# Optimization experiments

Measured on AMD Instinct MI355X. Metric: run time of the kernel, lower is better.

## Reference

```python
import jax, jax.numpy as jnp
import numpy as np

EPS = 1e-8
CUTOFF = 7.0
B, A, EPG = 128, 100, 2048
N, E = B * A, B * EPG
LAT, HID, FCH, NRBF, NTYPES, NT = 256, 128, 512, 16, 100, 50


def _lattice(lengths, angles):
    # pymatgen-style lattice_params_to_matrix; angles in degrees. -> [B,3,3] rows are a,b,c vectors
    a, b, c = lengths[:, 0], lengths[:, 1], lengths[:, 2]
    al, be, ga = (jnp.radians(angles[:, k]) for k in range(3))
    val = (jnp.cos(al) * jnp.cos(be) - jnp.cos(ga)) / (jnp.sin(al) * jnp.sin(be))
    gs = jnp.arccos(jnp.clip(val, -1.0, 1.0))
    z = jnp.zeros_like(a)
    va = jnp.stack([a * jnp.sin(be), z, a * jnp.cos(be)], -1)
    vb = jnp.stack([-b * jnp.sin(al) * jnp.cos(gs), b * jnp.sin(al) * jnp.sin(gs), b * jnp.cos(al)], -1)
    vc = jnp.stack([z, z, c], -1)
    return jnp.stack([va, vb, vc], 1)


def setup_inputs() -> dict:
    rng = np.random.default_rng(0)
    # sorted-per-graph edge list with i != j (so no_iden_mask is all-true)
    i = rng.integers(0, A, (B, EPG))
    j = (i + rng.integers(1, A, (B, EPG))) % A
    order = np.argsort(i * A + j, axis=1, kind='stable')
    i = np.take_along_axis(i, order, 1)
    j = np.take_along_axis(j, order, 1)
    goff = (np.arange(B) * A)[:, None]
    edge_index = np.stack([(j + goff).reshape(-1), (i + goff).reshape(-1)]).astype(np.int32)  # [2,E], row0=j(src), row1=i(dst)
    to_jimages = rng.integers(-1, 2, (E, 3)).astype(np.int32)
    batch = np.repeat(np.arange(B), A).astype(np.int32)
    num_atoms = np.full((B,), A, np.int32)
    atom_types = rng.integers(0, NTYPES, (N,)).astype(np.int32)
    time_steps = rng.integers(0, NT, (B,)).astype(np.int32)

    ks = jax.random.split(jax.random.key(0), 12)
    f32 = jnp.float32
    inp = dict(
        latents=jax.random.normal(ks[0], (B, LAT), f32),
        gt_frac_coords=jax.random.uniform(ks[1], (N, 3), f32),
        lengths=8.0 + 4.0 * jax.random.uniform(ks[2], (B, 3), f32),
        angles=90.0 + 8.0 * (jax.random.uniform(ks[3], (B, 3), f32) - 0.5),
        coord_noise=jax.random.normal(ks[4], (N, 3), f32),
        sigmas=jnp.exp(jnp.linspace(np.log(0.01), np.log(10.0), NT)).astype(f32),
        atom_emb=jax.random.normal(ks[5], (NTYPES, HID), f32),
        rbf_W=0.05 * jax.random.normal(ks[6], (NRBF, HID), f32),
        rbf_b=jnp.zeros((HID,), f32),
        bb_W=0.1 * jax.random.normal(ks[7], (HID, HID), f32),
        bb_b=jnp.zeros((HID,), f32),
        sc_W0=0.05 * jax.random.normal(ks[8], (LAT + HID, FCH), f32),
        sc_b0=jnp.zeros((FCH,), f32),
        sc_W1=0.05 * jax.random.normal(ks[9], (FCH, FCH), f32),
        sc_b1=jnp.zeros((FCH,), f32),
        sc_W2=0.05 * jax.random.normal(ks[10], (FCH, 1), f32),
        sc_b2=jnp.zeros((1,), f32),
        num_atoms=jnp.asarray(num_atoms),
        atom_types=jnp.asarray(atom_types),
        batch=jnp.asarray(batch),
        edge_index=jnp.asarray(edge_index),
        to_jimages=jnp.asarray(to_jimages),
        time_steps=jnp.asarray(time_steps),
    )
    return inp


def reference(latents, gt_frac_coords, lengths, angles, coord_noise, sigmas,
              atom_emb, rbf_W, rbf_b, bb_W, bb_b,
              sc_W0, sc_b0, sc_W1, sc_b1, sc_W2, sc_b2,
              num_atoms, atom_types, batch, edge_index, to_jimages, time_steps):
    seg_sum = jax.ops.segment_sum
    L = _lattice(lengths, angles)            # [B,3,3]
    Linv = jnp.linalg.inv(L)
    Ln, Lni = L[batch], Linv[batch]          # per-node lattice [N,3,3]
    cart_gt = jnp.einsum('ni,nij->nj', gt_frac_coords, Ln)
    sig_node = sigmas[time_steps][batch][:, None]              # [N,1]
    pert = cart_gt + sig_node * coord_noise
    # correct_cart_coords: wrap back into unit cell
    frac_p = jnp.einsum('ni,nij->nj', pert, Lni) % 1.0
    pert = jnp.einsum('ni,nij->nj', frac_p, Ln)
    jn, iN = edge_index[0], edge_index[1]
    offs = jnp.einsum('ei,eij->ej', to_jimages.astype(pert.dtype), L[batch[jn]])
    dvec = pert[iN] - pert[jn] - offs                           # [E,3]
    dist = jnp.linalg.norm(dvec, axis=-1)
    # backbone: atom-type embeddings + Gaussian RBF edge MLP -> [E,HID]
    mus = jnp.linspace(0.0, CUTOFF, rbf_W.shape[0]).astype(pert.dtype)
    rbf = jnp.exp(-10.0 * (dist[:, None] - mus) ** 2)
    h = atom_emb[atom_types]
    ef = jax.nn.silu((h[jn] + h[iN] + rbf @ rbf_W + rbf_b) @ bb_W + bb_b)
    # latents repeat_interleave(num_multi_edge_per_graph) == gather by edge's graph id
    ef = jnp.concatenate([ef, latents[batch[jn]]], axis=1)      # [E, HID+LAT]
    hh = jax.nn.relu(ef @ sc_W0 + sc_b0)
    hh = jax.nn.relu(hh @ sc_W1 + sc_b1)
    scores = hh @ sc_W2 + sc_b2                                 # [E,1]
    # align_gt_cart_coords: minimum-image gt coords relative to perturbed coords
    frac_gt = jnp.einsum('ni,nij->nj', cart_gt, Lni)
    fd = frac_gt - frac_p
    fd = fd - jnp.round(fd)
    aligned = pert + jnp.einsum('ni,nij->nj', fd, Ln)
    gt_dvec = aligned[iN] - aligned[jn] - offs
    gt_d = jnp.linalg.norm(gt_dvec, axis=-1, keepdims=True)
    pd = dist[:, None]
    gt_scores = gt_d - pd
    # per_node loss: group multi-edges by contiguous (i,j) runs
    start = jnp.concatenate([jnp.ones((1,), bool), (iN[1:] != iN[:-1]) | (jn[1:] != jn[:-1])])
    seg = jnp.cumsum(start.astype(jnp.int32)) - 1               # [E], < E segments
    cnt = seg_sum(jnp.ones((E,), pert.dtype), seg, num_segments=E)
    c = jnp.maximum(cnt, 1.0)
    sv = scores * dvec / (pd + EPS)
    gv = gt_scores * dvec / (pd + EPS)
    sE = seg_sum(sv, seg, num_segments=E) / c[:, None]
    gE = seg_sum(gv, seg, num_segments=E) / c[:, None]
    recv = jnp.round(seg_sum(iN.astype(pert.dtype), seg, num_segments=E) / c).astype(jnp.int32)
    sN = seg_sum(sE, recv, num_segments=N)                      # scores_per_node_pos [N,3]
    gN = seg_sum(gE, recv, num_segments=N)
    sq = (sN - gN / sig_node) ** 2
    na = num_atoms.astype(pert.dtype)[:, None]
    score_loss = (seg_sum(sq, batch, num_segments=B) / na).mean()
    # pbc symmetry regularizer
    preds = pert + sN / sig_node
    center = seg_sum(preds, batch, num_segments=B) / na
    dc = preds - center[batch]
    pbs = (jnp.abs(dc[:, 0].max() + dc[:, 0].min())
           + jnp.abs(dc[:, 1].max() + dc[:, 1].min())
           + jnp.abs(dc[:, 2].max() + dc[:, 2].min()))
    return (score_loss, pbs)
```

## Files before the change

kernel.cpp:

```cpp
#include <hip/hip_runtime.h>
#include <hip/hip_bf16.h>

namespace {
constexpr int Bb = 128, Nn = 12800, Ee = 262144;
constexpr int LAT = 256, HID = 128, FCH = 512, NRBF = 16;
constexpr int TE = 64;
constexpr int TSTRIDE = 1040;

constexpr int WS_L      = 0;
constexpr int WS_LI     = 1152;
constexpr int WS_SIG    = 2304;
constexpr int WS_RBFW2  = 2432;
constexpr int WS_CVEC   = 4480;
constexpr int WS_HB     = 4608;
constexpr int WS_LATP   = 17408;
constexpr int WS_PERT   = 82944;
constexpr int WS_ALIGN  = 121344;
constexpr int WS_SN     = 159744;
constexpr int WS_GN     = 198144;
constexpr int WS_PREDS  = 236544;
constexpr int WS_BSUM   = 274944;
constexpr int WS_CENTER = 275328;
constexpr int WS_MINMAX = 275712;
constexpr int WS_W0T_F  = 276000;
constexpr int WS_W1T_F  = 308768;
}

typedef short bf16x8 __attribute__((ext_vector_type(8)));
typedef float f32x4 __attribute__((ext_vector_type(4)));

static __device__ __forceinline__ unsigned short f2bf(float f) {
  unsigned int u = __float_as_uint(f);
  unsigned int r = (u + 0x7fffu + ((u >> 16) & 1u)) >> 16;
  return (unsigned short)r;
}
static __device__ __forceinline__ unsigned int pk2bf(float a, float b) {
  unsigned int r;
  asm("v_cvt_pk_bf16_f32 %0, %1, %2" : "=v"(r) : "v"(a), "v"(b));
  return r;
}
static __device__ __forceinline__ float fastrcp(float x) {
  return __builtin_amdgcn_rcpf(x);
}

static __device__ __forceinline__ void atomicMaxFloat(float* addr, float val) {
  int* ai = reinterpret_cast<int*>(addr);
  int old = *ai;
  while (__int_as_float(old) < val) {
    int assumed = old;
    old = atomicCAS(ai, assumed, __float_as_int(val));
    if (old == assumed) break;
  }
}
static __device__ __forceinline__ void atomicMinFloat(float* addr, float val) {
  int* ai = reinterpret_cast<int*>(addr);
  int old = *ai;
  while (__int_as_float(old) > val) {
    int assumed = old;
    old = atomicCAS(ai, assumed, __float_as_int(val));
    if (old == assumed) break;
  }
}

__global__ __launch_bounds__(256) void k_pre(
    const float* lengths, const float* angles, const float* sigmas, const int* tsteps,
    const float* aemb, const float* bbW, const float* rbfW, const float* rbfb,
    const float* bbb, const float* latents, const float* scW0, const float* scb0,
    const float* scW1, unsigned short* w0t, unsigned short* w1t, float* ws) {
  const int blk = blockIdx.x, t = threadIdx.x;
  if (blk < 304) {
    int gid = blk * 256 + t;
    if (gid < 2 * Nn * 3) ws[WS_SN + gid] = 0.f;
    else if (gid < 2 * Nn * 3 + 2 * Bb * 3) ws[WS_BSUM + (gid - 2 * Nn * 3)] = 0.f;
    else if (gid < 2 * Nn * 3 + 2 * Bb * 3 + 3) ws[WS_MINMAX + (gid - 2 * Nn * 3 - 2 * Bb * 3)] = -3.0e38f;
    else if (gid < 2 * Nn * 3 + 2 * Bb * 3 + 6) ws[WS_MINMAX + (gid - 2 * Nn * 3 - 2 * Bb * 3)] = 3.0e38f;
  } else if (blk == 304) {
    int b = t;
    if (b >= Bb) return;
    float a = lengths[b * 3 + 0], bl = lengths[b * 3 + 1], c = lengths[b * 3 + 2];
    const float d2r = 0.017453292519943295f;
    float al = angles[b * 3 + 0] * d2r, be = angles[b * 3 + 1] * d2r, ga = angles[b * 3 + 2] * d2r;
    float ca = cosf(al), cb = cosf(be), cg = cosf(ga), sa = sinf(al), sb = sinf(be);
    float val = (ca * cb - cg) / (sa * sb);
    val = fminf(1.f, fmaxf(-1.f, val));
    float gs = acosf(val);
    float L[3][3];
    L[0][0] = a * sb;              L[0][1] = 0.f;                L[0][2] = a * cb;
    L[1][0] = -bl * sa * cosf(gs); L[1][1] = bl * sa * sinf(gs); L[1][2] = bl * ca;
    L[2][0] = 0.f;                 L[2][1] = 0.f;                L[2][2] = c;
    float det = L[0][0] * (L[1][1] * L[2][2] - L[1][2] * L[2][1])
              - L[0][1] * (L[1][0] * L[2][2] - L[1][2] * L[2][0])
              + L[0][2] * (L[1][0] * L[2][1] - L[1][1] * L[2][0]);
    float id = 1.f / det;
    float inv[3][3];
    inv[0][0] =  (L[1][1]*L[2][2] - L[1][2]*L[2][1]) * id;
    inv[0][1] = -(L[0][1]*L[2][2] - L[0][2]*L[2][1]) * id;
    inv[0][2] =  (L[0][1]*L[1][2] - L[0][2]*L[1][1]) * id;
    inv[1][0] = -(L[1][0]*L[2][2] - L[1][2]*L[2][0]) * id;
    inv[1][1] =  (L[0][0]*L[2][2] - L[0][2]*L[2][0]) * id;
    inv[1][2] = -(L[0][0]*L[1][2] - L[0][2]*L[1][0]) * id;
    inv[2][0] =  (L[1][0]*L[2][1] - L[1][1]*L[2][0]) * id;
    inv[2][1] = -(L[0][0]*L[2][1] - L[0][1]*L[2][0]) * id;
    inv[2][2] =  (L[0][0]*L[1][1] - L[0][1]*L[1][0]) * id;
    for (int i = 0; i < 3; ++i)
      for (int j = 0; j < 3; ++j) {
        ws[WS_L + b * 9 + i * 3 + j] = L[i][j];
        ws[WS_LI + b * 9 + i * 3 + j] = inv[i][j];
      }
    ws[WS_SIG + b] = sigmas[tsteps[b]];
  } else if (blk < 405) {
    int tile = blk - 305;
    if (t < HID) {
      float acc = 0.f;
      for (int k = 0; k < HID; ++k) acc += aemb[tile * HID + k] * bbW[k * HID + t];
      ws[WS_HB + tile * HID + t] = acc;
    }
  } else if (blk == 405) {
    if (t < HID) {
      float accs[NRBF];
#pragma unroll
      for (int k = 0; k < NRBF; ++k) accs[k] = 0.f;
      float accb = 0.f;
      for (int m = 0; m < HID; ++m) {
        float w = bbW[m * HID + t];
#pragma unroll
        for (int k = 0; k < NRBF; ++k) accs[k] += rbfW[k * HID + m] * w;
        accb += rbfb[m] * w;
      }
#pragma unroll
      for (int k = 0; k < NRBF; ++k) ws[WS_RBFW2 + k * HID + t] = accs[k];
      ws[WS_CVEC + t] = accb + bbb[t];
    }
  } else if (blk < 534) {
    int b = blk - 406;
    __shared__ float lat[LAT];
    lat[t] = latents[b * LAT + t];
    __syncthreads();
    int c0 = 2 * t;
    float a0 = 0.f, a1 = 0.f;
    for (int m = 0; m < LAT; ++m) {
      float2 w = *reinterpret_cast<const float2*>(scW0 + (HID + m) * FCH + c0);
      float lm = lat[m];
      a0 += lm * w.x;
      a1 += lm * w.y;
    }
    ws[WS_LATP + b * FCH + c0] = a0 + scb0[c0];
    ws[WS_LATP + b * FCH + c0 + 1] = a1 + scb0[c0 + 1];
  } else if (blk < 790) {
    int tid = (blk - 534) * 256 + t;
    int col = tid & 511, k = tid >> 9;
    int id = (((col >> 4) * 4 + (k >> 5)) * 64 + ((k & 31) >> 3) * 16 + (col & 15)) * 8 + (k & 7);
    w0t[id] = f2bf(scW0[tid]);
  } else {
    int tid = (blk - 790) * 256 + t;
    int col = tid & 511, k = tid >> 9;
    int id = (((col >> 4) * 16 + (k >> 5)) * 64 + ((k & 31) >> 3) * 16 + (col & 15)) * 8 + (k & 7);
    w1t[id] = f2bf(scW1[tid]);
  }
}

__global__ void k_node(const float* frac, const float* noise, const int* batch, float* ws) {
  int n = blockIdx.x * blockDim.x + threadIdx.x;
  if (n >= Nn) return;
  int b = batch[n];
  float L[9], Li[9];
#pragma unroll
  for (int i = 0; i < 9; ++i) { L[i] = ws[WS_L + b * 9 + i]; Li[i] = ws[WS_LI + b * 9 + i]; }
  float f0 = frac[n * 3], f1 = frac[n * 3 + 1], f2 = frac[n * 3 + 2];
  float cg[3], p0[3], fp[3], pe[3], fg[3], fd[3];
#pragma unroll
  for (int j = 0; j < 3; ++j) cg[j] = f0 * L[j] + f1 * L[3 + j] + f2 * L[6 + j];
  float sig = ws[WS_SIG + b];
#pragma unroll
  for (int j = 0; j < 3; ++j) p0[j] = cg[j] + sig * noise[n * 3 + j];
#pragma unroll
  for (int j = 0; j < 3; ++j) {
    float v = p0[0] * Li[j] + p0[1] * Li[3 + j] + p0[2] * Li[6 + j];
    fp[j] = v - floorf(v);
  }
#pragma unroll
  for (int j = 0; j < 3; ++j) pe[j] = fp[0] * L[j] + fp[1] * L[3 + j] + fp[2] * L[6 + j];
#pragma unroll
  for (int j = 0; j < 3; ++j) fg[j] = cg[0] * Li[j] + cg[1] * Li[3 + j] + cg[2] * Li[6 + j];
#pragma unroll
  for (int j = 0; j < 3; ++j) { float d = fg[j] - fp[j]; fd[j] = d - rintf(d); }
#pragma unroll
  for (int j = 0; j < 3; ++j) {
    ws[WS_PERT + n * 3 + j] = pe[j];
    ws[WS_ALIGN + n * 3 + j] = pe[j] + fd[0] * L[j] + fd[1] * L[3 + j] + fd[2] * L[6 + j];
  }
}

__global__ __launch_bounds__(512, 4) void k_edge(
    const int* ei, const int* toj, const int* batch, const int* atype,
    const unsigned short* w0t, const unsigned short* w1t,
    const float* scb1, const float* scW2, const float* scb2, float* ws) {
  __shared__ __align__(16) char s_hh_b[64 * TSTRIDE];
  __shared__ float s_dvec[TE][3];
  __shared__ float s_dist[TE], s_gtd[TE];
  __shared__ int s_tj[TE], s_ti[TE];
  __shared__ float s_wsum[8][TE];

  char* s_ef_b = s_hh_b;
  float* s_rbfw2 = (float*)(s_hh_b + 16640);
  float* s_cvec  = (float*)(s_hh_b + 24832);
  float* s_rbfE  = (float*)(s_hh_b + 25344);

  const int t = threadIdx.x;
  const int e0 = blockIdx.x * TE;
  const int b0 = batch[ei[e0]];

  {
    const float4* src = (const float4*)(ws + WS_RBFW2);
    float4* dst = (float4*)s_rbfw2;
    dst[t] = src[t];
    if (t < 32) ((float4*)s_cvec)[t] = ((const float4*)(ws + WS_CVEC))[t];
  }
  if (t < TE) {
    int e = e0 + t;
    int jn = ei[e], iN = ei[Ee + e];
    int b = batch[jn];
    float tx = (float)toj[e * 3], ty = (float)toj[e * 3 + 1], tz = (float)toj[e * 3 + 2];
    const float* L = ws + WS_L + b * 9;
    float dv[3], gv[3];
#pragma unroll
    for (int j = 0; j < 3; ++j) {
      float off = tx * L[j] + ty * L[3 + j] + tz * L[6 + j];
      dv[j] = ws[WS_PERT + iN * 3 + j] - ws[WS_PERT + jn * 3 + j] - off;
      gv[j] = ws[WS_ALIGN + iN * 3 + j] - ws[WS_ALIGN + jn * 3 + j] - off;
    }
    float dist = sqrtf(dv[0] * dv[0] + dv[1] * dv[1] + dv[2] * dv[2]);
    float gtd = sqrtf(gv[0] * gv[0] + gv[1] * gv[1] + gv[2] * gv[2]);
#pragma unroll
    for (int j = 0; j < 3; ++j) s_dvec[t][j] = dv[j];
    s_dist[t] = dist;
    s_gtd[t] = gtd;
    s_tj[t] = atype[jn]; s_ti[t] = atype[iN];
    const float step = 7.0f / 15.0f;
#pragma unroll
    for (int k = 0; k < NRBF; ++k) {
      float d = dist - (float)k * step;
      s_rbfE[t * NRBF + k] = __expf(-10.f * d * d);
    }
  }
  __syncthreads();

  {
    int e = t >> 3;
    int c0 = (t & 7) * 16;
    int tj = s_tj[e], ti = s_ti[e];
    float4 rb4[4];
#pragma unroll
    for (int q = 0; q < 4; ++q) rb4[q] = ((const float4*)(s_rbfE + e * NRBF))[q];
    float rb[NRBF] = {rb4[0].x, rb4[0].y, rb4[0].z, rb4[0].w,
                      rb4[1].x, rb4[1].y, rb4[1].z, rb4[1].w,
                      rb4[2].x, rb4[2].y, rb4[2].z, rb4[2].w,
                      rb4[3].x, rb4[3].y, rb4[3].z, rb4[3].w};
    float4 z4[4];
#pragma unroll
    for (int q = 0; q < 4; ++q) {
      float4 a = *(const float4*)(ws + WS_HB + tj * HID + c0 + q * 4);
      float4 bq = *(const float4*)(ws + WS_HB + ti * HID + c0 + q * 4);
      float4 cv = ((const float4*)s_cvec)[c0 / 4 + q];
      z4[q].x = a.x + bq.x + cv.x; z4[q].y = a.y + bq.y + cv.y;
      z4[q].z = a.z + bq.z + cv.z; z4[q].w = a.w + bq.w + cv.w;
    }
#pragma unroll
    for (int k = 0; k < NRBF; ++k) {
      float rbk = rb[k];
#pragma unroll
      for (int q = 0; q < 4; ++q) {
        float4 wv4 = ((const float4*)s_rbfw2)[k * 32 + c0 / 4 + q];
        z4[q].x += rbk * wv4.x; z4[q].y += rbk * wv4.y;
        z4[q].z += rbk * wv4.z; z4[q].w += rbk * wv4.w;
      }
    }
    float sv[16];
#pragma unroll
    for (int q = 0; q < 4; ++q) {
      sv[q * 4 + 0] = z4[q].x * fastrcp(1.f + __expf(-z4[q].x));
      sv[q * 4 + 1] = z4[q].y * fastrcp(1.f + __expf(-z4[q].y));
      sv[q * 4 + 2] = z4[q].z * fastrcp(1.f + __expf(-z4[q].z));
      sv[q * 4 + 3] = z4[q].w * fastrcp(1.f + __expf(-z4[q].w));
    }
    unsigned int w[8];
#pragma unroll
    for (int p = 0; p < 8; ++p) w[p] = pk2bf(sv[2 * p], sv[2 * p + 1]);
    int eT = e >> 4, el = e & 15;
#pragma unroll
    for (int o = 0; o < 2; ++o) {
      int hid = c0 + 8 * o;
      int kt = hid >> 5;
      int oct = (hid & 31) >> 3;
      int addr = (kt * 4 + eT) * TSTRIDE + (el + 16 * oct) * 16;
      uint4 val = {w[4 * o + 0], w[4 * o + 1], w[4 * o + 2], w[4 * o + 3]};
      *(uint4*)(s_ef_b + addr) = val;
    }
  }
  __syncthreads();

  const int lane = t & 63;
  const int wv = t >> 6;
  const int el = lane & 15;
  const int q  = lane >> 4;

  {
    f32x4 acc[4][4];
#pragma unroll
    for (int m = 0; m < 4; ++m)
#pragma unroll
      for (int n = 0; n < 4; ++n) acc[m][n] = (f32x4){0.f, 0.f, 0.f, 0.f};
    const unsigned short* w0base = w0t + (size_t)(wv * 4) * 4 * 512 + lane * 8;
#pragma unroll
    for (int kt = 0; kt < 4; ++kt) {
      bf16x8 aw[4];
#pragma unroll
      for (int m = 0; m < 4; ++m)
        aw[m] = *(const bf16x8*)(w0base + (size_t)(m * 4 + kt) * 512);
      bf16x8 bf[4];
#pragma unroll
      for (int n = 0; n < 4; ++n)
        bf[n] = *(const bf16x8*)(s_ef_b + (kt * 4 + n) * TSTRIDE + lane * 16);
      __builtin_amdgcn_s_setprio(1);
#pragma unroll
      for (int n = 0; n < 4; ++n)
#pragma unroll
        for (int m = 0; m < 4; ++m)
          acc[m][n] = __builtin_amdgcn_mfma_f32_16x16x32_bf16(aw[m], bf[n], acc[m][n], 0, 0, 0);
      __builtin_amdgcn_s_setprio(0);
    }
    __syncthreads();
#pragma unroll
    for (int m = 0; m < 4; ++m) {
      float4 lp = *(const float4*)(ws + WS_LATP + b0 * FCH + wv * 64 + m * 16 + q * 4);
#pragma unroll
      for (int n = 0; n < 4; ++n) {
        f32x4 v = acc[m][n];
        float h0 = fmaxf(v[0] + lp.x, 0.f);
        float h1 = fmaxf(v[1] + lp.y, 0.f);
        float h2 = fmaxf(v[2] + lp.z, 0.f);
        float h3 = fmaxf(v[3] + lp.w, 0.f);
        uint2 val = {pk2bf(h0, h1), pk2bf(h2, h3)};
        int kT = wv * 2 + (m >> 1);
        int oct = (m & 1) * 2 + (q >> 1);
        int addr = (kT * 4 + n) * TSTRIDE + (el + 16 * oct) * 16 + (q & 1) * 8;
        *(uint2*)(s_hh_b + addr) = val;
      }
    }
  }
  __syncthreads();

  {
    f32x4 acc[4][4];
#pragma unroll
    for (int m = 0; m < 4; ++m)
#pragma unroll
      for (int n = 0; n < 4; ++n) acc[m][n] = (f32x4){0.f, 0.f, 0.f, 0.f};
    const unsigned short* w1base = w1t + (size_t)(wv * 4) * 16 * 512 + lane * 8;
#pragma unroll 4
    for (int kt = 0; kt < 16; ++kt) {
      bf16x8 aw[4];
#pragma unroll
      for (int m = 0; m < 4; ++m)
        aw[m] = *(const bf16x8*)(w1base + (size_t)(m * 16 + kt) * 512);
      bf16x8 bf[4];
#pragma unroll
      for (int n = 0; n < 4; ++n)
        bf[n] = *(const bf16x8*)(s_hh_b + (kt * 4 + n) * TSTRIDE + lane * 16);
      __builtin_amdgcn_s_setprio(1);
#pragma unroll
      for (int n = 0; n < 4; ++n)
#pragma unroll
        for (int m = 0; m < 4; ++m)
          acc[m][n] = __builtin_amdgcn_mfma_f32_16x16x32_bf16(aw[m], bf[n], acc[m][n], 0, 0, 0);
      __builtin_amdgcn_s_setprio(0);
    }
    float p[4] = {0.f, 0.f, 0.f, 0.f};
#pragma unroll
    for (int m = 0; m < 4; ++m) {
      int colb = wv * 64 + m * 16 + q * 4;
      float4 b1v = *(const float4*)(scb1 + colb);
      float4 w2v = *(const float4*)(scW2 + colb);
#pragma unroll
      for (int n = 0; n < 4; ++n) {
        f32x4 v = acc[m][n];
        p[n] += fmaxf(v[0] + b1v.x, 0.f) * w2v.x;
        p[n] += fmaxf(v[1] + b1v.y, 0.f) * w2v.y;
        p[n] += fmaxf(v[2] + b1v.z, 0.f) * w2v.z;
        p[n] += fmaxf(v[3] + b1v.w, 0.f) * w2v.w;
      }
    }
#pragma unroll
    for (int n = 0; n < 4; ++n) {
      float x = p[n];
      x += __shfl_xor(x, 16);
      x += __shfl_xor(x, 32);
      p[n] = x;
    }
    if (lane < 16) {
#pragma unroll
      for (int n = 0; n < 4; ++n) s_wsum[wv][n * 16 + el] = p[n];
    }
  }
  __syncthreads();

  if (t < TE) {
    int e = e0 + t;
    float score = scb2[0];
#pragma unroll
    for (int w = 0; w < 8; ++w) score += s_wsum[w][t];
    int jn = ei[e], iN = ei[Ee + e];
    int s = e;
    while (s > 0 && ei[s - 1] == jn && ei[Ee + s - 1] == iN) --s;
    int en = e;
    while (en + 1 < Ee && ei[en + 1] == jn && ei[Ee + en + 1] == iN) ++en;
    float invc = fastrcp((float)(en - s + 1));
    float dist = s_dist[t];
    float rden = fastrcp(dist + 1e-8f);
    float gts = s_gtd[t] - dist;
#pragma unroll
    for (int j = 0; j < 3; ++j) {
      float dir = s_dvec[t][j] * rden;
      atomicAdd(&ws[WS_SN + iN * 3 + j], score * dir * invc);
      atomicAdd(&ws[WS_GN + iN * 3 + j], gts * dir * invc);
    }
  }
}

__global__ void k_node2(const int* batch, float* ws) {
  int n = blockIdx.x * blockDim.x + threadIdx.x;
  if (n >= Nn) return;
  int b = batch[n];
  float sig = ws[WS_SIG + b];
#pragma unroll
  for (int j = 0; j < 3; ++j) {
    float s = ws[WS_SN + n * 3 + j], g = ws[WS_GN + n * 3 + j];
    float d = s - g / sig;
    atomicAdd(&ws[WS_BSUM + b * 3 + j], d * d);
    float pr = ws[WS_PERT + n * 3 + j] + s / sig;
    ws[WS_PREDS + n * 3 + j] = pr;
    atomicAdd(&ws[WS_CENTER + b * 3 + j], pr);
  }
}

__global__ void k_minmax(const int* batch, const int* num_atoms, float* ws) {
  int n = blockIdx.x * blockDim.x + threadIdx.x;
  int lane = threadIdx.x & 63, wid = threadIdx.x >> 6;
  float mx[3], mn[3];
  if (n < Nn) {
    int b = batch[n];
    float na = (float)num_atoms[b];
#pragma unroll
    for (int j = 0; j < 3; ++j) {
      float v = ws[WS_PREDS + n * 3 + j] - ws[WS_CENTER + b * 3 + j] / na;
      mx[j] = v; mn[j] = v;
    }
  } else {
#pragma unroll
    for (int j = 0; j < 3; ++j) { mx[j] = -3.0e38f; mn[j] = 3.0e38f; }
  }
#pragma unroll
  for (int off = 32; off >= 1; off >>= 1) {
#pragma unroll
    for (int j = 0; j < 3; ++j) {
      mx[j] = fmaxf(mx[j], __shfl_xor(mx[j], off));
      mn[j] = fminf(mn[j], __shfl_xor(mn[j], off));
    }
  }
  __shared__ float smx[4][3], smn[4][3];
  if (lane == 0) {
#pragma unroll
    for (int j = 0; j < 3; ++j) { smx[wid][j] = mx[j]; smn[wid][j] = mn[j]; }
  }
  __syncthreads();
  if (threadIdx.x == 0) {
#pragma unroll
    for (int j = 0; j < 3; ++j) {
      float M = fmaxf(fmaxf(smx[0][j], smx[1][j]), fmaxf(smx[2][j], smx[3][j]));
      float m = fminf(fminf(smn[0][j], smn[1][j]), fminf(smn[2][j], smn[3][j]));
      atomicMaxFloat(&ws[WS_MINMAX + j], M);
      atomicMinFloat(&ws[WS_MINMAX + 3 + j], m);
    }
  }
}

__global__ void k_final(const int* num_atoms, const float* ws, float* out) {
  int t = threadIdx.x;
  float loss = 0.f;
  if (t < Bb) {
    float na = (float)num_atoms[t];
    loss = (ws[WS_BSUM + t * 3] + ws[WS_BSUM + t * 3 + 1] + ws[WS_BSUM + t * 3 + 2]) / na;
  }
#pragma unroll
  for (int off = 32; off >= 1; off >>= 1) loss += __shfl_xor(loss, off);
  __shared__ float s2[2];
  if ((t & 63) == 0) s2[t >> 6] = loss;
  __syncthreads();
  if (t == 0) {
    float L = (s2[0] + s2[1]) / (3.0f * (float)Bb);
    float pbs = fabsf(ws[WS_MINMAX + 0] + ws[WS_MINMAX + 3]) +
                fabsf(ws[WS_MINMAX + 1] + ws[WS_MINMAX + 4]) +
                fabsf(ws[WS_MINMAX + 2] + ws[WS_MINMAX + 5]);
    out[0] = L;
    out[1] = pbs;
  }
}

extern "C" void kernel_launch(void* const* d_in, const int* in_sizes, int n_in,
                              void* d_out, int out_size, void* d_ws, size_t ws_size,
                              hipStream_t stream) {
  const float* latents = (const float*)d_in[0];
  const float* gtf     = (const float*)d_in[1];
  const float* lengths = (const float*)d_in[2];
  const float* angles  = (const float*)d_in[3];
  const float* noise   = (const float*)d_in[4];
  const float* sigmas  = (const float*)d_in[5];
  const float* aemb    = (const float*)d_in[6];
  const float* rbfW    = (const float*)d_in[7];
  const float* rbfb    = (const float*)d_in[8];
  const float* bbW     = (const float*)d_in[9];
  const float* bbb     = (const float*)d_in[10];
  const float* scW0    = (const float*)d_in[11];
  const float* scb0    = (const float*)d_in[12];
  const float* scW1    = (const float*)d_in[13];
  const float* scb1    = (const float*)d_in[14];
  const float* scW2    = (const float*)d_in[15];
  const float* scb2    = (const float*)d_in[16];
  const int* num_atoms = (const int*)d_in[17];
  const int* atype     = (const int*)d_in[18];
  const int* batch     = (const int*)d_in[19];
  const int* ei        = (const int*)d_in[20];
  const int* toj       = (const int*)d_in[21];
  const int* tsteps    = (const int*)d_in[22];
  float* ws = (float*)d_ws;
  float* out = (float*)d_out;
  unsigned short* w0t = (unsigned short*)(ws + WS_W0T_F);
  unsigned short* w1t = (unsigned short*)(ws + WS_W1T_F);

  hipLaunchKernelGGL(k_pre, dim3(1814), dim3(256), 0, stream,
                     lengths, angles, sigmas, tsteps, aemb, bbW, rbfW, rbfb, bbb,
                     latents, scW0, scb0, scW1, w0t, w1t, ws);
  hipLaunchKernelGGL(k_node, dim3(50), dim3(256), 0, stream, gtf, noise, batch, ws);
  hipLaunchKernelGGL(k_edge, dim3(Ee / TE), dim3(512), 0, stream,
                     ei, toj, batch, atype, w0t, w1t, scb1, scW2, scb2, ws);
  hipLaunchKernelGGL(k_node2, dim3(50), dim3(256), 0, stream, batch, ws);
  hipLaunchKernelGGL(k_minmax, dim3(50), dim3(256), 0, stream, batch, num_atoms, ws);
  hipLaunchKernelGGL(k_final, dim3(1), dim3(128), 0, stream, num_atoms, ws, out);
}
```

Before: 323.0 us.

## Compute edge RBF projection with MFMA and fold node kernel into prep

The per-edge RBF-to-hidden projection (16 RBF features times a 16x128 weight) now runs on bf16 MFMA instructions using a prepacked bf16 weight tile, replacing the scalar FMA loop and the LDS staging of RBF values and weights. The node perturbation kernel is merged into the prep kernel, which recomputes the lattice per node so it no longer depends on an earlier block. Weight packing is rewritten so each thread writes 8 packed bf16 values instead of one. This cuts ALU work, a kernel launch and LDS traffic, at the cost of bf16 rounding in the RBF term and redundant lattice trigonometry per node.

```diff
diff --git a/kernel.cpp b/kernel.cpp
--- a/kernel.cpp
+++ b/kernel.cpp
@@ -22,11 +22,13 @@
 constexpr int WS_BSUM   = 274944;
 constexpr int WS_CENTER = 275328;
 constexpr int WS_MINMAX = 275712;
-constexpr int WS_W0T_F  = 276000;
-constexpr int WS_W1T_F  = 308768;
+constexpr int WS_W0T_F   = 276000;
+constexpr int WS_W1T_F   = 308768;
+constexpr int WS_RBFW2T_F = 439840;
 }
 
 typedef short bf16x8 __attribute__((ext_vector_type(8)));
+typedef unsigned short u16x8 __attribute__((ext_vector_type(8)));
 typedef float f32x4 __attribute__((ext_vector_type(4)));
 
 static __device__ __forceinline__ unsigned short f2bf(float f) {
@@ -41,6 +43,33 @@
 }
 static __device__ __forceinline__ float fastrcp(float x) {
   return __builtin_amdgcn_rcpf(x);
+}
+
+static __device__ __forceinline__ void make_lattice(
+    const float* lengths, const float* angles, int b, float L[9], float Li[9]) {
+  float a = lengths[b * 3 + 0], bl = lengths[b * 3 + 1], c = lengths[b * 3 + 2];
+  const float d2r = 0.017453292519943295f;
+  float al = angles[b * 3 + 0] * d2r, be = angles[b * 3 + 1] * d2r, ga = angles[b * 3 + 2] * d2r;
+  float ca = cosf(al), cb = cosf(be), cg = cosf(ga), sa = sinf(al), sb = sinf(be);
+  float val = (ca * cb - cg) / (sa * sb);
+  val = fminf(1.f, fmaxf(-1.f, val));
+  float gs = acosf(val);
+  L[0] = a * sb;              L[1] = 0.f;                L[2] = a * cb;
+  L[3] = -bl * sa * cosf(gs); L[4] = bl * sa * sinf(gs); L[5] = bl * ca;
+  L[6] = 0.f;                 L[7] = 0.f;                L[8] = c;
+  float det = L[0] * (L[4] * L[8] - L[5] * L[7])
+            - L[1] * (L[3] * L[8] - L[5] * L[6])
+            + L[2] * (L[3] * L[7] - L[4] * L[6]);
+  float id = 1.f / det;
+  Li[0] =  (L[4] * L[8] - L[5] * L[7]) * id;
+  Li[1] = -(L[1] * L[8] - L[2] * L[7]) * id;
+  Li[2] =  (L[1] * L[5] - L[2] * L[4]) * id;
+  Li[3] = -(L[3] * L[8] - L[5] * L[6]) * id;
+  Li[4] =  (L[0] * L[8] - L[2] * L[6]) * id;
+  Li[5] = -(L[0] * L[5] - L[2] * L[3]) * id;
+  Li[6] =  (L[3] * L[7] - L[4] * L[6]) * id;
+  Li[7] = -(L[0] * L[7] - L[1] * L[6]) * id;
+  Li[8] =  (L[0] * L[4] - L[1] * L[3]) * id;
 }
 
 static __device__ __forceinline__ void atomicMaxFloat(float* addr, float val) {
@@ -66,7 +95,9 @@
     const float* lengths, const float* angles, const float* sigmas, const int* tsteps,
     const float* aemb, const float* bbW, const float* rbfW, const float* rbfb,
     const float* bbb, const float* latents, const float* scW0, const float* scb0,
-    const float* scW1, unsigned short* w0t, unsigned short* w1t, float* ws) {
+    const float* scW1, const float* gtf, const float* noise, const int* batch,
+    const int* atype, unsigned short* w0t, unsigned short* w1t,
+    unsigned short* rbfw2t, float* ws) {
   const int blk = blockIdx.x, t = threadIdx.x;
   if (blk < 304) {
     int gid = blk * 256 + t;
@@ -77,36 +108,13 @@
   } else if (blk == 304) {
     int b = t;
     if (b >= Bb) return;
-    float a = lengths[b * 3 + 0], bl = lengths[b * 3 + 1], c = lengths[b * 3 + 2];
-    const float d2r = 0.017453292519943295f;
-    float al = angles[b * 3 + 0] * d2r, be = angles[b * 3 + 1] * d2r, ga = angles[b * 3 + 2] * d2r;
-    float ca = cosf(al), cb = cosf(be), cg = cosf(ga), sa = sinf(al), sb = sinf(be);
-    float val = (ca * cb - cg) / (sa * sb);
-    val = fminf(1.f, fmaxf(-1.f, val));
-    float gs = acosf(val);
-    float L[3][3];
-    L[0][0] = a * sb;              L[0][1] = 0.f;                L[0][2] = a * cb;
-    L[1][0] = -bl * sa * cosf(gs); L[1][1] = bl * sa * sinf(gs); L[1][2] = bl * ca;
-    L[2][0] = 0.f;                 L[2][1] = 0.f;                L[2][2] = c;
-    float det = L[0][0] * (L[1][1] * L[2][2] - L[1][2] * L[2][1])
-              - L[0][1] * (L[1][0] * L[2][2] - L[1][2] * L[2][0])
-              + L[0][2] * (L[1][0] * L[2][1] - L[1][1] * L[2][0]);
-    float id = 1.f / det;
-    float inv[3][3];
-    inv[0][0] =  (L[1][1]*L[2][2] - L[1][2]*L[2][1]) * id;
-    inv[0][1] = -(L[0][1]*L[2][2] - L[0][2]*L[2][1]) * id;
-    inv[0][2] =  (L[0][1]*L[1][2] - L[0][2]*L[1][1]) * id;
-    inv[1][0] = -(L[1][0]*L[2][2] - L[1][2]*L[2][0]) * id;
-    inv[1][1] =  (L[0][0]*L[2][2] - L[0][2]*L[2][0]) * id;
-    inv[1][2] = -(L[0][0]*L[1][2] - L[0][2]*L[1][0]) * id;
-    inv[2][0] =  (L[1][0]*L[2][1] - L[1][1]*L[2][0]) * id;
-    inv[2][1] = -(L[0][0]*L[2][1] - L[0][1]*L[2][0]) * id;
-    inv[2][2] =  (L[0][0]*L[1][1] - L[0][1]*L[1][0]) * id;
-    for (int i = 0; i < 3; ++i)
-      for (int j = 0; j < 3; ++j) {
-        ws[WS_L + b * 9 + i * 3 + j] = L[i][j];
-        ws[WS_LI + b * 9 + i * 3 + j] = inv[i][j];
-      }
+    float L[9], Li[9];
+    make_lattice(lengths, angles, b, L, Li);
+#pragma unroll
+    for (int i = 0; i < 9; ++i) {
+      ws[WS_L + b * 9 + i] = L[i];
+      ws[WS_LI + b * 9 + i] = Li[i];
+    }
     ws[WS_SIG + b] = sigmas[tsteps[b]];
   } else if (blk < 405) {
     int tile = blk - 305;
@@ -146,54 +154,81 @@
     }
     ws[WS_LATP + b * FCH + c0] = a0 + scb0[c0];
     ws[WS_LATP + b * FCH + c0 + 1] = a1 + scb0[c0 + 1];
-  } else if (blk < 790) {
-    int tid = (blk - 534) * 256 + t;
-    int col = tid & 511, k = tid >> 9;
-    int id = (((col >> 4) * 4 + (k >> 5)) * 64 + ((k & 31) >> 3) * 16 + (col & 15)) * 8 + (k & 7);
-    w0t[id] = f2bf(scW0[tid]);
+  } else if (blk < 566) {
+    int id8 = (blk - 534) * 256 + t;
+    int tile = id8 >> 6, lf = id8 & 63;
+    int colTile = tile >> 2, kTile = tile & 3;
+    int col = colTile * 16 + (lf & 15);
+    int kbase = kTile * 32 + (lf >> 4) * 8;
+    u16x8 v;
+#pragma unroll
+    for (int e = 0; e < 8; ++e) v[e] = f2bf(scW0[(kbase + e) * FCH + col]);
+    *(u16x8*)(w0t + id8 * 8) = v;
+  } else if (blk < 694) {
+    int id8 = (blk - 566) * 256 + t;
+    int tile = id8 >> 6, lf = id8 & 63;
+    int colTile = tile >> 4, kTile = tile & 15;
+    int col = colTile * 16 + (lf & 15);
+    int kbase = kTile * 32 + (lf >> 4) * 8;
+    u16x8 v;
+#pragma unroll
+    for (int e = 0; e < 8; ++e) v[e] = f2bf(scW1[(kbase + e) * FCH + col]);
+    *(u16x8*)(w1t + id8 * 8) = v;
+  } else if (blk < 696) {
+    int id = (blk - 694) * 256 + t;
+    if (id < 512) {
+      int tile = id >> 6, lf = id & 63;
+      int c = tile * 16 + (lf & 15);
+      u16x8 v;
+#pragma unroll
+      for (int e = 0; e < 8; ++e) {
+        int k = (lf >> 4) * 8 + e;
+        if (k < NRBF) {
+          float acc = 0.f;
+          for (int m = 0; m < HID; ++m) acc += rbfW[k * HID + m] * bbW[m * HID + c];
+          v[e] = f2bf(acc);
+        } else {
+          v[e] = 0;
+        }
+      }
+      *(u16x8*)(rbfw2t + id * 8) = v;
+    }
   } else {
-    int tid = (blk - 790) * 256 + t;
-    int col = tid & 511, k = tid >> 9;
-    int id = (((col >> 4) * 16 + (k >> 5)) * 64 + ((k & 31) >> 3) * 16 + (col & 15)) * 8 + (k & 7);
-    w1t[id] = f2bf(scW1[tid]);
-  }
-}
-
-__global__ void k_node(const float* frac, const float* noise, const int* batch, float* ws) {
-  int n = blockIdx.x * blockDim.x + threadIdx.x;
-  if (n >= Nn) return;
-  int b = batch[n];
-  float L[9], Li[9];
-#pragma unroll
-  for (int i = 0; i < 9; ++i) { L[i] = ws[WS_L + b * 9 + i]; Li[i] = ws[WS_LI + b * 9 + i]; }
-  float f0 = frac[n * 3], f1 = frac[n * 3 + 1], f2 = frac[n * 3 + 2];
-  float cg[3], p0[3], fp[3], pe[3], fg[3], fd[3];
-#pragma unroll
-  for (int j = 0; j < 3; ++j) cg[j] = f0 * L[j] + f1 * L[3 + j] + f2 * L[6 + j];
-  float sig = ws[WS_SIG + b];
-#pragma unroll
-  for (int j = 0; j < 3; ++j) p0[j] = cg[j] + sig * noise[n * 3 + j];
-#pragma unroll
-  for (int j = 0; j < 3; ++j) {
-    float v = p0[0] * Li[j] + p0[1] * Li[3 + j] + p0[2] * Li[6 + j];
-    fp[j] = v - floorf(v);
-  }
-#pragma unroll
-  for (int j = 0; j < 3; ++j) pe[j] = fp[0] * L[j] + fp[1] * L[3 + j] + fp[2] * L[6 + j];
-#pragma unroll
-  for (int j = 0; j < 3; ++j) fg[j] = cg[0] * Li[j] + cg[1] * Li[3 + j] + cg[2] * Li[6 + j];
-#pragma unroll
-  for (int j = 0; j < 3; ++j) { float d = fg[j] - fp[j]; fd[j] = d - rintf(d); }
-#pragma unroll
-  for (int j = 0; j < 3; ++j) {
-    ws[WS_PERT + n * 3 + j] = pe[j];
-    ws[WS_ALIGN + n * 3 + j] = pe[j] + fd[0] * L[j] + fd[1] * L[3 + j] + fd[2] * L[6 + j];
+    int n = (blk - 696) * 256 + t;
+    if (n >= Nn) return;
+    int b = batch[n];
+    float L[9], Li[9];
+    make_lattice(lengths, angles, b, L, Li);
+    float sig = sigmas[tsteps[b]];
+    float f0 = gtf[n * 3], f1 = gtf[n * 3 + 1], f2 = gtf[n * 3 + 2];
+    float cg[3], p0[3], fp[3], pe[3], fg[3], fd[3];
+#pragma unroll
+    for (int j = 0; j < 3; ++j) cg[j] = f0 * L[j] + f1 * L[3 + j] + f2 * L[6 + j];
+#pragma unroll
+    for (int j = 0; j < 3; ++j) p0[j] = cg[j] + sig * noise[n * 3 + j];
+#pragma unroll
+    for (int j = 0; j < 3; ++j) {
+      float v = p0[0] * Li[j] + p0[1] * Li[3 + j] + p0[2] * Li[6 + j];
+      fp[j] = v - floorf(v);
+    }
+#pragma unroll
+    for (int j = 0; j < 3; ++j) pe[j] = fp[0] * L[j] + fp[1] * L[3 + j] + fp[2] * L[6 + j];
+#pragma unroll
+    for (int j = 0; j < 3; ++j) fg[j] = cg[0] * Li[j] + cg[1] * Li[3 + j] + cg[2] * Li[6 + j];
+#pragma unroll
+    for (int j = 0; j < 3; ++j) { float d = fg[j] - fp[j]; fd[j] = d - rintf(d); }
+#pragma unroll
+    for (int j = 0; j < 3; ++j) {
+      ws[WS_PERT + n * 3 + j] = pe[j];
+      ws[WS_ALIGN + n * 3 + j] = pe[j] + fd[0] * L[j] + fd[1] * L[3 + j] + fd[2] * L[6 + j];
+    }
   }
 }
 
 __global__ __launch_bounds__(512, 4) void k_edge(
     const int* ei, const int* toj, const int* batch, const int* atype,
     const unsigned short* w0t, const unsigned short* w1t,
+    const unsigned short* rbfw2t,
     const float* scb1, const float* scW2, const float* scb2, float* ws) {
   __shared__ __align__(16) char s_hh_b[64 * TSTRIDE];
   __shared__ float s_dvec[TE][3];
@@ -202,20 +237,16 @@
   __shared__ float s_wsum[8][TE];
 
   char* s_ef_b = s_hh_b;
-  float* s_rbfw2 = (float*)(s_hh_b + 16640);
-  float* s_cvec  = (float*)(s_hh_b + 24832);
-  float* s_rbfE  = (float*)(s_hh_b + 25344);
 
   const int t = threadIdx.x;
   const int e0 = blockIdx.x * TE;
   const int b0 = batch[ei[e0]];
 
-  {
-    const float4* src = (const float4*)(ws + WS_RBFW2);
-    float4* dst = (float4*)s_rbfw2;
-    dst[t] = src[t];
-    if (t < 32) ((float4*)s_cvec)[t] = ((const float4*)(ws + WS_CVEC))[t];
-  }
+  const int lane = t & 63;
+  const int wv = t >> 6;
+  const int el = lane & 15;
+  const int q  = lane >> 4;
+
   if (t < TE) {
     int e = e0 + t;
     int jn = ei[e], iN = ei[Ee + e];
@@ -236,73 +267,62 @@
     s_dist[t] = dist;
     s_gtd[t] = gtd;
     s_tj[t] = atype[jn]; s_ti[t] = atype[iN];
+  }
+  __syncthreads();
+
+  {
+    bf16x8 arb = *(const bf16x8*)(rbfw2t + wv * 512 + lane * 8);
     const float step = 7.0f / 15.0f;
-#pragma unroll
-    for (int k = 0; k < NRBF; ++k) {
-      float d = dist - (float)k * step;
-      s_rbfE[t * NRBF + k] = __expf(-10.f * d * d);
+    bf16x8 brb[4];
+#pragma unroll
+    for (int n = 0; n < 4; ++n) {
+      float d = s_dist[n * 16 + el];
+      unsigned int wb0 = 0, wb1 = 0, wb2 = 0, wb3 = 0;
+      if (q < 2) {
+        float kbase = (float)(8 * q) * step;
+        float d0 = d - kbase;
+#pragma unroll
+        for (int p = 0; p < 4; ++p) {
+          float m0 = d0 - (float)(2 * p) * step;
+          float m1 = m0 - step;
+          unsigned int r = pk2bf(__expf(-10.f * m0 * m0), __expf(-10.f * m1 * m1));
+          if (p == 0) wb0 = r; else if (p == 1) wb1 = r;
+          else if (p == 2) wb2 = r; else wb3 = r;
+        }
+      }
+      uint4 u = {wb0, wb1, wb2, wb3};
+      brb[n] = *reinterpret_cast<bf16x8*>(&u);
+    }
+    f32x4 accB[4];
+#pragma unroll
+    for (int n = 0; n < 4; ++n)
+      accB[n] = __builtin_amdgcn_mfma_f32_16x16x32_bf16(
+          arb, brb[n], (f32x4){0.f, 0.f, 0.f, 0.f}, 0, 0, 0);
+    int col0 = wv * 16 + q * 4;
+    float4 cv = *(const float4*)(ws + WS_CVEC + col0);
+    int kT = wv >> 1;
+    int oct = (wv & 1) * 2 + (q >> 1);
+#pragma unroll
+    for (int n = 0; n < 4; ++n) {
+      int eg = n * 16 + el;
+      int tj = s_tj[eg], ti = s_ti[eg];
+      float4 hj = *(const float4*)(ws + WS_HB + tj * HID + col0);
+      float4 hi = *(const float4*)(ws + WS_HB + ti * HID + col0);
+      f32x4 a = accB[n];
+      float z0 = a[0] + hj.x + hi.x + cv.x;
+      float z1 = a[1] + hj.y + hi.y + cv.y;
+      float z2 = a[2] + hj.z + hi.z + cv.z;
+      float z3 = a[3] + hj.w + hi.w + cv.w;
+      float s0 = z0 * fastrcp(1.f + __expf(-z0));
+      float s1 = z1 * fastrcp(1.f + __expf(-z1));
+      float s2 = z2 * fastrcp(1.f + __expf(-z2));
+      float s3 = z3 * fastrcp(1.f + __expf(-z3));
+      uint2 val = {pk2bf(s0, s1), pk2bf(s2, s3)};
+      int addr = (kT * 4 + n) * TSTRIDE + (el + 16 * oct) * 16 + (q & 1) * 8;
+      *(uint2*)(s_ef_b + addr) = val;
     }
   }
   __syncthreads();
-
-  {
-    int e = t >> 3;
-    int c0 = (t & 7) * 16;
-    int tj = s_tj[e], ti = s_ti[e];
-    float4 rb4[4];
-#pragma unroll
-    for (int q = 0; q < 4; ++q) rb4[q] = ((const float4*)(s_rbfE + e * NRBF))[q];
-    float rb[NRBF] = {rb4[0].x, rb4[0].y, rb4[0].z, rb4[0].w,
-                      rb4[1].x, rb4[1].y, rb4[1].z, rb4[1].w,
-                      rb4[2].x, rb4[2].y, rb4[2].z, rb4[2].w,
-                      rb4[3].x, rb4[3].y, rb4[3].z, rb4[3].w};
-    float4 z4[4];
-#pragma unroll
-    for (int q = 0; q < 4; ++q) {
-      float4 a = *(const float4*)(ws + WS_HB + tj * HID + c0 + q * 4);
-      float4 bq = *(const float4*)(ws + WS_HB + ti * HID + c0 + q * 4);
-      float4 cv = ((const float4*)s_cvec)[c0 / 4 + q];
-      z4[q].x = a.x + bq.x + cv.x; z4[q].y = a.y + bq.y + cv.y;
-      z4[q].z = a.z + bq.z + cv.z; z4[q].w = a.w + bq.w + cv.w;
-    }
-#pragma unroll
-    for (int k = 0; k < NRBF; ++k) {
-      float rbk = rb[k];
-#pragma unroll
-      for (int q = 0; q < 4; ++q) {
-        float4 wv4 = ((const float4*)s_rbfw2)[k * 32 + c0 / 4 + q];
-        z4[q].x += rbk * wv4.x; z4[q].y += rbk * wv4.y;
-        z4[q].z += rbk * wv4.z; z4[q].w += rbk * wv4.w;
-      }
-    }
-    float sv[16];
-#pragma unroll
-    for (int q = 0; q < 4; ++q) {
-      sv[q * 4 + 0] = z4[q].x * fastrcp(1.f + __expf(-z4[q].x));
-      sv[q * 4 + 1] = z4[q].y * fastrcp(1.f + __expf(-z4[q].y));
-      sv[q * 4 + 2] = z4[q].z * fastrcp(1.f + __expf(-z4[q].z));
-      sv[q * 4 + 3] = z4[q].w * fastrcp(1.f + __expf(-z4[q].w));
-    }
-    unsigned int w[8];
-#pragma unroll
-    for (int p = 0; p < 8; ++p) w[p] = pk2bf(sv[2 * p], sv[2 * p + 1]);
-    int eT = e >> 4, el = e & 15;
-#pragma unroll
-    for (int o = 0; o < 2; ++o) {
-      int hid = c0 + 8 * o;
-      int kt = hid >> 5;
-      int oct = (hid & 31) >> 3;
-      int addr = (kt * 4 + eT) * TSTRIDE + (el + 16 * oct) * 16;
-      uint4 val = {w[4 * o + 0], w[4 * o + 1], w[4 * o + 2], w[4 * o + 3]};
-      *(uint4*)(s_ef_b + addr) = val;
-    }
-  }
-  __syncthreads();
-
-  const int lane = t & 63;
-  const int wv = t >> 6;
-  const int el = lane & 15;
-  const int q  = lane >> 4;
 
   {
     f32x4 acc[4][4];
@@ -536,13 +556,14 @@
   float* out = (float*)d_out;
   unsigned short* w0t = (unsigned short*)(ws + WS_W0T_F);
   unsigned short* w1t = (unsigned short*)(ws + WS_W1T_F);
-
-  hipLaunchKernelGGL(k_pre, dim3(1814), dim3(256), 0, stream,
+  unsigned short* rbfw2t = (unsigned short*)(ws + WS_RBFW2T_F);
+
+  hipLaunchKernelGGL(k_pre, dim3(746), dim3(256), 0, stream,
                      lengths, angles, sigmas, tsteps, aemb, bbW, rbfW, rbfb, bbb,
-                     latents, scW0, scb0, scW1, w0t, w1t, ws);
-  hipLaunchKernelGGL(k_node, dim3(50), dim3(256), 0, stream, gtf, noise, batch, ws);
+                     latents, scW0, scb0, scW1, gtf, noise, batch, atype,
+                     w0t, w1t, rbfw2t, ws);
   hipLaunchKernelGGL(k_edge, dim3(Ee / TE), dim3(512), 0, stream,
-                     ei, toj, batch, atype, w0t, w1t, scb1, scW2, scb2, ws);
+                     ei, toj, batch, atype, w0t, w1t, rbfw2t, scb1, scW2, scb2, ws);
   hipLaunchKernelGGL(k_node2, dim3(50), dim3(256), 0, stream, batch, ws);
   hipLaunchKernelGGL(k_minmax, dim3(50), dim3(256), 0, stream, batch, num_atoms, ws);
   hipLaunchKernelGGL(k_final, dim3(1), dim3(128), 0, stream, num_atoms, ws, out);
```

New measurement: 315.3 us. 1.02x faster.
